# Performance work log

Hardware: AMD Instinct MI355X
Metric: run time of the kernel (lower is better)

## Reference

```python
import jax, jax.numpy as jnp
import numpy as np

N = 100_000   # number of sparse points
C = 128       # channels
K3 = 27       # 3x3x3 kernel offsets


def sparse_conv(x, nbr, W, b):
    """Minkowski-style sparse conv: gather-GEMM-scatter.
    x:   [N, Cin] point features
    nbr: [N, K3] neighbor index per kernel offset; index N -> missing (zero row)
    W:   [K3, Cin, Cout], b: [Cout]
    """
    x_pad = jnp.concatenate([x, jnp.zeros((1, x.shape[1]), x.dtype)], axis=0)

    def step(acc, wk_nk):
        Wk, nk = wk_nk                      # Wk: [Cin,Cout], nk: [N]
        return acc + x_pad[nk] @ Wk, None   # gather + GEMM, accumulate

    acc0 = jnp.broadcast_to(b, (x.shape[0], W.shape[2])).astype(x.dtype)
    acc, _ = jax.lax.scan(step, acc0, (W, nbr.T))
    return acc


def setup_inputs() -> dict:
    key = jax.random.key(0)
    ks = jax.random.split(key, 12)
    Ch = C // 2

    def w(k, shape, fan_in):
        return jax.random.normal(k, shape, dtype=jnp.float32) / np.sqrt(fan_in)

    x = jax.random.normal(ks[0], (N, C), dtype=jnp.float32)
    # neighbor map; value N means "no neighbor" (maps to zero-padded row)
    nbr = jax.random.randint(ks[1], (N, K3), 0, N + 1, dtype=jnp.int32)

    return {
        "x": x,
        "nbr": nbr,
        "W00": w(ks[2], (K3, C, Ch), K3 * C),   # conv0_0: kxkxk, C -> C/2
        "b00": jnp.zeros((Ch,), jnp.float32),
        "W01": w(ks[3], (K3, Ch, Ch), K3 * Ch),  # conv0_1: kxkxk, C/2 -> C/2
        "b01": jnp.zeros((Ch,), jnp.float32),
        "W10": w(ks[4], (C, Ch), C),             # conv1_0: 1x1x1, C -> C/2
        "b10": jnp.zeros((Ch,), jnp.float32),
        "W11": w(ks[5], (K3, Ch, Ch), K3 * Ch),  # conv1_1: kxkxk, C/2 -> C/2
        "b11": jnp.zeros((Ch,), jnp.float32),
        "W12": w(ks[6], (Ch, Ch), Ch),           # conv1_2: 1x1x1, C/2 -> C/2
        "b12": jnp.zeros((Ch,), jnp.float32),
    }


def reference(x, nbr, W00, b00, W01, b01, W10, b10, W11, b11, W12, b12):
    # branch 0: conv -> relu -> conv
    h0 = jax.nn.relu(sparse_conv(x, nbr, W00, b00))
    out0 = sparse_conv(h0, nbr, W01, b01)
    # branch 1: 1x1 conv -> relu -> conv -> relu -> 1x1 conv
    h1 = jax.nn.relu(x @ W10 + b10)
    h1 = jax.nn.relu(sparse_conv(h1, nbr, W11, b11))
    out1 = h1 @ W12 + b12
    # concat channels, residual add
    return jnp.concatenate([out0, out1], axis=1) + x
```

## Files before the change

kernel.cpp:

```cpp
#include <hip/hip_runtime.h>
#include <hip/hip_bf16.h>
#include <stdint.h>

typedef __bf16 bf16x8 __attribute__((ext_vector_type(8)));
typedef float  f32x4  __attribute__((ext_vector_type(4)));

#define MFMA(A, B, C) __builtin_amdgcn_mfma_f32_16x16x32_bf16((A), (B), (C), 0, 0, 0)

#define LDS_BARRIER() asm volatile("s_waitcnt lgkmcnt(0)\n\ts_barrier" ::: "memory")

static __device__ __forceinline__ unsigned short f2b(float f) {
    union { float f; unsigned int u; } v; v.f = f;
    return (unsigned short)((v.u + 0x7FFFu + ((v.u >> 16) & 1u)) >> 16);
}

static __device__ __forceinline__ bf16x8 perm_frag(int sel, bf16x8 D) {
    union { bf16x8 v; int d[4]; } u, r;
    u.v = D;
#pragma unroll
    for (int w = 0; w < 4; ++w) r.d[w] = __builtin_amdgcn_ds_bpermute(sel, u.d[w]);
    return r.v;
}

__global__ __launch_bounds__(256) void convert_kernel(
    const float* __restrict__ x, unsigned short* __restrict__ xb,
    unsigned short* __restrict__ hb, int N) {
    long long i = (long long)blockIdx.x * blockDim.x + threadIdx.x;
    long long base = i * 4;
    long long nx = (long long)N * 128;
    long long total = nx + 128;
    if (base >= total) return;
    if (base < nx) {
        float4 v = *(const float4*)(x + base);
        ushort4 o;
        o.x = f2b(v.x); o.y = f2b(v.y); o.z = f2b(v.z); o.w = f2b(v.w);
        *(ushort4*)(xb + base) = o;
    } else {
        ushort4 z = make_ushort4(0, 0, 0, 0);
        *(ushort4*)(xb + base) = z;
        *(ushort4*)(hb + base) = z;
    }
}

__global__ __launch_bounds__(256) void pack_kernel(
    const float* __restrict__ W00, const float* __restrict__ W01,
    const float* __restrict__ W10, const float* __restrict__ W11,
    const float* __restrict__ W12,
    unsigned short* __restrict__ wp00, unsigned short* __restrict__ wpC,
    unsigned short* __restrict__ wp10, unsigned short* __restrict__ wp12) {
    int g = blockIdx.x * blockDim.x + threadIdx.x;
    const float* W; int cinSteps; int which;
    if (g < 27648)      { W = W00; cinSteps = 4; which = 0; }
    else if (g < 41472) { g -= 27648; W = W01; cinSteps = 2; which = 1; }
    else if (g < 55296) { g -= 41472; W = W11; cinSteps = 2; which = 2; }
    else if (g < 56320) { g -= 55296; W = W10; cinSteps = 4; which = 3; }
    else if (g < 56832) { g -= 56320; W = W12; cinSteps = 2; which = 4; }
    else return;
    int lane = g & 63;
    int st   = g >> 6;
    int t    = st & 3;
    int s    = st >> 2;
    int q = lane >> 4, n16 = lane & 15;
    int k    = s / cinSteps;
    int cinb = (s % cinSteps) * 32;
    int Cin  = cinSteps * 32;
    int cout = t * 16 + n16;
    unsigned short o[8];
#pragma unroll
    for (int j = 0; j < 8; ++j) {
        float v = W[(size_t)(k * Cin + cinb + q * 8 + j) * 64 + cout];
        o[j] = f2b(v);
    }
    unsigned short* dst;
    if (which == 0)      dst = wp00 + (size_t)g * 8;
    else if (which == 1) dst = wpC + (size_t)k * 8192 +
                               ((size_t)(((s & 1) * 4 + t) * 64 + lane)) * 8;
    else if (which == 2) dst = wpC + (size_t)k * 8192 + 4096 +
                               ((size_t)(((s & 1) * 4 + t) * 64 + lane)) * 8;
    else if (which == 3) dst = wp10 + (size_t)g * 8;
    else                 dst = wp12 + (size_t)g * 8;
    *(ushort4*)(dst)     = make_ushort4(o[0], o[1], o[2], o[3]);
    *(ushort4*)(dst + 4) = make_ushort4(o[4], o[5], o[6], o[7]);
}

__global__ __launch_bounds__(256, 2) void passB_kernel(
    const unsigned short* __restrict__ xb, const int* __restrict__ nbr,
    const unsigned short* __restrict__ wp00, const unsigned short* __restrict__ wp10,
    const float* __restrict__ b00, const float* __restrict__ b10,
    unsigned short* __restrict__ hb, int N, int* __restrict__ ctr, int nstrips) {
    __shared__ __align__(16) unsigned short bbuf[2][8192];
    __shared__ int lds_idx[128 * 27];
    __shared__ int sstrip;
    int tid = threadIdx.x;
    int lane = tid & 63;
    int wv   = tid >> 6;
    int q = lane >> 4, n16 = lane & 15;
    int rowq = lane >> 2, chunk = lane & 3;
    int sel = (n16 * 4 + q) * 4;

    for (;;) {
        if (tid == 0) sstrip = atomicAdd(ctr, 1);
        __syncthreads();
        int strip = sstrip;
        if (strip >= nstrips) break;
        int rowbase = strip * 128 + wv * 32;

        int4 br[4];
#pragma unroll
        for (int j = 0; j < 4; ++j) br[j] = *(const int4*)(wp00 + j * 2048 + tid * 8);
        {
            long long gbase = (long long)strip * 128 * 27;
            long long lim = (long long)N * 27 - 1;
            for (int i = tid; i < 3456; i += 256) {
                long long gi = gbase + i; if (gi > lim) gi = lim;
                lds_idx[i] = nbr[gi];
            }
        }
#pragma unroll
        for (int j = 0; j < 4; ++j) *(int4*)(&bbuf[0][j * 2048 + tid * 8]) = br[j];
        __syncthreads();

        f32x4 acc0[2][4];
        f32x4 acc1[2][4];
#pragma unroll
        for (int rs = 0; rs < 2; ++rs)
#pragma unroll
            for (int t = 0; t < 4; ++t) { acc0[rs][t] = (f32x4)0.f; acc1[rs][t] = (f32x4)0.f; }

        int idxb0 = (wv * 32 + rowq) * 27;
        int idxb1 = (wv * 32 + 16 + rowq) * 27;
        int own0 = min(rowbase + rowq, N - 1);
        int own1 = min(rowbase + 16 + rowq, N - 1);

        int ia = lds_idx[idxb0], ib = lds_idx[idxb1];
        bf16x8 D0[4], D1[4];
        {
            const unsigned short* p0 = xb + (size_t)ia * 128 + chunk * 8;
            const unsigned short* p1 = xb + (size_t)ib * 128 + chunk * 8;
#pragma unroll
            for (int s2 = 0; s2 < 4; ++s2) {
                D0[s2] = *(const bf16x8*)(p0 + s2 * 32);
                D1[s2] = *(const bf16x8*)(p1 + s2 * 32);
            }
        }

        for (int k = 0; k < 27; ++k) {
            int buf = k & 1;
            if (k < 26) {
                const unsigned short* src = wp00 + (size_t)(k + 1) * 8192;
#pragma unroll
                for (int j = 0; j < 4; ++j) br[j] = *(const int4*)(src + j * 2048 + tid * 8);
            }
            int ian = (k + 1 < 27) ? lds_idx[idxb0 + k + 1] : own0;
            int ibn = (k + 1 < 27) ? lds_idx[idxb1 + k + 1] : own1;
            bf16x8 D0n[4], D1n[4];
            {
                const unsigned short* p0 = xb + (size_t)ian * 128 + chunk * 8;
                const unsigned short* p1 = xb + (size_t)ibn * 128 + chunk * 8;
#pragma unroll
                for (int s2 = 0; s2 < 4; ++s2) {
                    D0n[s2] = *(const bf16x8*)(p0 + s2 * 32);
                    D1n[s2] = *(const bf16x8*)(p1 + s2 * 32);
                }
            }
            const unsigned short* lb = &bbuf[buf][0];
#pragma unroll
            for (int s2 = 0; s2 < 4; ++s2) {
                bf16x8 A0 = perm_frag(sel, D0[s2]);
                bf16x8 A1 = perm_frag(sel, D1[s2]);
#pragma unroll
                for (int t = 0; t < 4; ++t) {
                    bf16x8 B = *(const bf16x8*)(lb + (s2 * 4 + t) * 512 + lane * 8);
                    acc0[0][t] = MFMA(A0, B, acc0[0][t]);
                    acc0[1][t] = MFMA(A1, B, acc0[1][t]);
                }
            }
            if (k < 26) {
#pragma unroll
                for (int j = 0; j < 4; ++j)
                    *(int4*)(&bbuf[buf ^ 1][j * 2048 + tid * 8]) = br[j];
            }
#pragma unroll
            for (int s2 = 0; s2 < 4; ++s2) { D0[s2] = D0n[s2]; D1[s2] = D1n[s2]; }
            LDS_BARRIER();
        }

#pragma unroll
        for (int s2 = 0; s2 < 4; ++s2) {
            bf16x8 A0 = perm_frag(sel, D0[s2]);
            bf16x8 A1 = perm_frag(sel, D1[s2]);
#pragma unroll
            for (int t = 0; t < 4; ++t) {
                bf16x8 B = *(const bf16x8*)(wp10 + s2 * 2048 + t * 512 + lane * 8);
                acc1[0][t] = MFMA(A0, B, acc1[0][t]);
                acc1[1][t] = MFMA(A1, B, acc1[1][t]);
            }
        }

#pragma unroll
        for (int rs = 0; rs < 2; ++rs)
#pragma unroll
            for (int t = 0; t < 4; ++t) {
                int col = t * 16 + n16;
                float bb0 = b00[col], bb1 = b10[col];
#pragma unroll
                for (int r = 0; r < 4; ++r) {
                    int row = rowbase + rs * 16 + q * 4 + r;
                    if (row < N) {
                        hb[(size_t)row * 128 + col]      = f2b(fmaxf(acc0[rs][t][r] + bb0, 0.f));
                        hb[(size_t)row * 128 + 64 + col] = f2b(fmaxf(acc1[rs][t][r] + bb1, 0.f));
                    }
                }
            }
        __syncthreads();
    }
}

__global__ __launch_bounds__(256, 2) void passC_kernel(
    const unsigned short* __restrict__ hb, const int* __restrict__ nbr,
    const float* __restrict__ x,
    const unsigned short* __restrict__ wpC, const unsigned short* __restrict__ wp12,
    const float* __restrict__ b01, const float* __restrict__ b11,
    const float* __restrict__ b12, float* __restrict__ out, int N,
    int* __restrict__ ctr, int nstrips) {
    __shared__ __align__(16) unsigned short bbuf[2][8192];
    __shared__ int lds_idx[128 * 27];
    __shared__ int sstrip;
    int tid = threadIdx.x;
    int lane = tid & 63;
    int wv   = tid >> 6;
    int q = lane >> 4, n16 = lane & 15;
    int rowq = lane >> 2, chunk = lane & 3;
    int sel = (n16 * 4 + q) * 4;

    for (;;) {
        if (tid == 0) sstrip = atomicAdd(ctr, 1);
        __syncthreads();
        int strip = sstrip;
        if (strip >= nstrips) break;
        int rowbase = strip * 128 + wv * 32;

        int4 br[4];
#pragma unroll
        for (int j = 0; j < 4; ++j) br[j] = *(const int4*)(wpC + j * 2048 + tid * 8);
        {
            long long gbase = (long long)strip * 128 * 27;
            long long lim = (long long)N * 27 - 1;
            for (int i = tid; i < 3456; i += 256) {
                long long gi = gbase + i; if (gi > lim) gi = lim;
                lds_idx[i] = nbr[gi];
            }
        }
#pragma unroll
        for (int j = 0; j < 4; ++j) *(int4*)(&bbuf[0][j * 2048 + tid * 8]) = br[j];
        __syncthreads();

        f32x4 accO0[2][4];
        f32x4 accT[2][4];
#pragma unroll
        for (int rs = 0; rs < 2; ++rs)
#pragma unroll
            for (int t = 0; t < 4; ++t) { accO0[rs][t] = (f32x4)0.f; accT[rs][t] = (f32x4)0.f; }

        int idxb0 = (wv * 32 + rowq) * 27;
        int idxb1 = (wv * 32 + 16 + rowq) * 27;

        int ia = lds_idx[idxb0], ib = lds_idx[idxb1];
        bf16x8 DA0[2], DC0[2], DA1[2], DC1[2];
        {
            const unsigned short* p0 = hb + (size_t)ia * 128 + chunk * 8;
            const unsigned short* p1 = hb + (size_t)ib * 128 + chunk * 8;
#pragma unroll
            for (int s2 = 0; s2 < 2; ++s2) {
                DA0[s2] = *(const bf16x8*)(p0 + s2 * 32);
                DC0[s2] = *(const bf16x8*)(p0 + 64 + s2 * 32);
                DA1[s2] = *(const bf16x8*)(p1 + s2 * 32);
                DC1[s2] = *(const bf16x8*)(p1 + 64 + s2 * 32);
            }
        }

        for (int k = 0; k < 27; ++k) {
            int buf = k & 1;
            if (k < 26) {
                const unsigned short* src = wpC + (size_t)(k + 1) * 8192;
#pragma unroll
                for (int j = 0; j < 4; ++j) br[j] = *(const int4*)(src + j * 2048 + tid * 8);
            }
            bf16x8 DA0n[2], DC0n[2], DA1n[2], DC1n[2];
            if (k < 26) {
                int ian = lds_idx[idxb0 + k + 1];
                int ibn = lds_idx[idxb1 + k + 1];
                const unsigned short* p0 = hb + (size_t)ian * 128 + chunk * 8;
                const unsigned short* p1 = hb + (size_t)ibn * 128 + chunk * 8;
#pragma unroll
                for (int s2 = 0; s2 < 2; ++s2) {
                    DA0n[s2] = *(const bf16x8*)(p0 + s2 * 32);
                    DC0n[s2] = *(const bf16x8*)(p0 + 64 + s2 * 32);
                    DA1n[s2] = *(const bf16x8*)(p1 + s2 * 32);
                    DC1n[s2] = *(const bf16x8*)(p1 + 64 + s2 * 32);
                }
            }
            const unsigned short* lb = &bbuf[buf][0];
#pragma unroll
            for (int s2 = 0; s2 < 2; ++s2) {
                bf16x8 A0 = perm_frag(sel, DA0[s2]);
                bf16x8 A1 = perm_frag(sel, DA1[s2]);
#pragma unroll
                for (int t = 0; t < 4; ++t) {
                    bf16x8 B = *(const bf16x8*)(lb + (s2 * 4 + t) * 512 + lane * 8);
                    accO0[0][t] = MFMA(A0, B, accO0[0][t]);
                    accO0[1][t] = MFMA(A1, B, accO0[1][t]);
                }
                bf16x8 C0 = perm_frag(sel, DC0[s2]);
                bf16x8 C1 = perm_frag(sel, DC1[s2]);
#pragma unroll
                for (int t = 0; t < 4; ++t) {
                    bf16x8 B2 = *(const bf16x8*)(lb + 4096 + (s2 * 4 + t) * 512 + lane * 8);
                    accT[0][t] = MFMA(C0, B2, accT[0][t]);
                    accT[1][t] = MFMA(C1, B2, accT[1][t]);
                }
            }
            if (k < 26) {
#pragma unroll
                for (int j = 0; j < 4; ++j)
                    *(int4*)(&bbuf[buf ^ 1][j * 2048 + tid * 8]) = br[j];
#pragma unroll
                for (int s2 = 0; s2 < 2; ++s2) {
                    DA0[s2] = DA0n[s2]; DC0[s2] = DC0n[s2];
                    DA1[s2] = DA1n[s2]; DC1[s2] = DC1n[s2];
                }
            }
            LDS_BARRIER();
        }

        unsigned short* scratch = &bbuf[0][0];
        unsigned short* myl = scratch + wv * 2304;
#pragma unroll
        for (int rs = 0; rs < 2; ++rs)
#pragma unroll
            for (int t = 0; t < 4; ++t) {
                int col = t * 16 + n16;
                float bo = b01[col], bt = b11[col];
#pragma unroll
                for (int r = 0; r < 4; ++r) {
                    int row = rowbase + rs * 16 + q * 4 + r;
                    if (row < N) {
                        float xv = __builtin_nontemporal_load(x + (size_t)row * 128 + col);
                        __builtin_nontemporal_store(accO0[rs][t][r] + bo + xv,
                                                    out + (size_t)row * 128 + col);
                    }
                    float tv = fmaxf(accT[rs][t][r] + bt, 0.f);
                    myl[(rs * 16 + q * 4 + r) * 72 + col] = f2b(tv);
                }
            }

        f32x4 accO1[2][4];
#pragma unroll
        for (int rs = 0; rs < 2; ++rs)
#pragma unroll
            for (int t = 0; t < 4; ++t) accO1[rs][t] = (f32x4)0.f;
#pragma unroll
        for (int s2 = 0; s2 < 2; ++s2) {
            bf16x8 A0 = *(const bf16x8*)(myl + n16 * 72 + s2 * 32 + q * 8);
            bf16x8 A1 = *(const bf16x8*)(myl + (16 + n16) * 72 + s2 * 32 + q * 8);
#pragma unroll
            for (int t = 0; t < 4; ++t) {
                bf16x8 B = *(const bf16x8*)(wp12 + s2 * 2048 + t * 512 + lane * 8);
                accO1[0][t] = MFMA(A0, B, accO1[0][t]);
                accO1[1][t] = MFMA(A1, B, accO1[1][t]);
            }
        }
#pragma unroll
        for (int rs = 0; rs < 2; ++rs)
#pragma unroll
            for (int t = 0; t < 4; ++t) {
                int col = t * 16 + n16;
                float bo = b12[col];
#pragma unroll
                for (int r = 0; r < 4; ++r) {
                    int row = rowbase + rs * 16 + q * 4 + r;
                    if (row < N) {
                        float xv = __builtin_nontemporal_load(x + (size_t)row * 128 + 64 + col);
                        __builtin_nontemporal_store(accO1[rs][t][r] + bo + xv,
                                                    out + (size_t)row * 128 + 64 + col);
                    }
                }
            }
        __syncthreads();
    }
}

extern "C" void kernel_launch(void* const* d_in, const int* in_sizes, int n_in,
                              void* d_out, int out_size, void* d_ws, size_t ws_size,
                              hipStream_t stream) {
    const float* x   = (const float*)d_in[0];
    const int*   nbr = (const int*)d_in[1];
    const float* W00 = (const float*)d_in[2];
    const float* b00 = (const float*)d_in[3];
    const float* W01 = (const float*)d_in[4];
    const float* b01 = (const float*)d_in[5];
    const float* W10 = (const float*)d_in[6];
    const float* b10 = (const float*)d_in[7];
    const float* W11 = (const float*)d_in[8];
    const float* b11 = (const float*)d_in[9];
    const float* W12 = (const float*)d_in[10];
    const float* b12 = (const float*)d_in[11];
    float* out = (float*)d_out;
    int N = in_sizes[0] / 128;

    char* ws = (char*)d_ws;
    size_t cur = 0;
    unsigned short* xb  = (unsigned short*)(ws + cur); cur += (size_t)(N + 1) * 128 * 2;
    unsigned short* hb  = (unsigned short*)(ws + cur); cur += (size_t)(N + 1) * 128 * 2;
    unsigned short* wp00 = (unsigned short*)(ws + cur); cur += 27648 * 8 * 2;
    unsigned short* wpC  = (unsigned short*)(ws + cur); cur += (size_t)27 * 8192 * 2;
    unsigned short* wp10 = (unsigned short*)(ws + cur); cur += 8192 * 2;
    unsigned short* wp12 = (unsigned short*)(ws + cur); cur += 4096 * 2;
    cur = (cur + 255) & ~(size_t)255;
    int* ctrs = (int*)(ws + cur); cur += 256;

    hipMemsetAsync(ctrs, 0, 8, stream);
    long long cvt_groups = ((long long)N * 128 + 128) / 4;
    int cvt_blocks = (int)((cvt_groups + 255) / 256);
    convert_kernel<<<cvt_blocks, 256, 0, stream>>>(x, xb, hb, N);
    pack_kernel<<<222, 256, 0, stream>>>(W00, W01, W10, W11, W12,
                                         wp00, wpC, wp10, wp12);
    int nstrips = (N + 127) / 128;
    passB_kernel<<<768, 256, 0, stream>>>(xb, nbr, wp00, wp10, b00, b10, hb, N,
                                          ctrs + 0, nstrips);
    passC_kernel<<<768, 256, 0, stream>>>(hb, nbr, x, wpC, wp12,
                                          b01, b11, b12, out, N,
                                          ctrs + 1, nstrips);
}
```

Measured before the change: 414.4 us.

## Drop persistent atomic scheduler, use one block per strip, remove bpermute shuffles

Replaces the persistent-block work queue (atomic counter plus memset) with a plain grid of one block per 128-row strip, and raises launch bounds to 3 blocks per CU. Each lane now gathers neighbor rows directly in the MFMA A-operand layout (row = n16, k-chunk = q), so the ds_bpermute fragment shuffles are no longer needed. This cuts per-iteration LDS permute traffic and the scheduler overhead. The cost is that each 16-lane group now reads 16 different rows per load, giving less contiguous gathers and more blocks to launch, and the tighter register budget could cause spills.

```diff
diff --git a/kernel.cpp b/kernel.cpp
--- a/kernel.cpp
+++ b/kernel.cpp
@@ -12,14 +12,6 @@
 static __device__ __forceinline__ unsigned short f2b(float f) {
     union { float f; unsigned int u; } v; v.f = f;
     return (unsigned short)((v.u + 0x7FFFu + ((v.u >> 16) & 1u)) >> 16);
-}
-
-static __device__ __forceinline__ bf16x8 perm_frag(int sel, bf16x8 D) {
-    union { bf16x8 v; int d[4]; } u, r;
-    u.v = D;
-#pragma unroll
-    for (int w = 0; w < 4; ++w) r.d[w] = __builtin_amdgcn_ds_bpermute(sel, u.d[w]);
-    return r.v;
 }
 
 __global__ __launch_bounds__(256) void convert_kernel(
@@ -83,311 +75,280 @@
     *(ushort4*)(dst + 4) = make_ushort4(o[4], o[5], o[6], o[7]);
 }
 
-__global__ __launch_bounds__(256, 2) void passB_kernel(
+__global__ __launch_bounds__(256, 3) void passB_kernel(
     const unsigned short* __restrict__ xb, const int* __restrict__ nbr,
     const unsigned short* __restrict__ wp00, const unsigned short* __restrict__ wp10,
     const float* __restrict__ b00, const float* __restrict__ b10,
-    unsigned short* __restrict__ hb, int N, int* __restrict__ ctr, int nstrips) {
+    unsigned short* __restrict__ hb, int N) {
     __shared__ __align__(16) unsigned short bbuf[2][8192];
     __shared__ int lds_idx[128 * 27];
-    __shared__ int sstrip;
-    int tid = threadIdx.x;
-    int lane = tid & 63;
-    int wv   = tid >> 6;
-    int q = lane >> 4, n16 = lane & 15;
-    int rowq = lane >> 2, chunk = lane & 3;
-    int sel = (n16 * 4 + q) * 4;
-
-    for (;;) {
-        if (tid == 0) sstrip = atomicAdd(ctr, 1);
-        __syncthreads();
-        int strip = sstrip;
-        if (strip >= nstrips) break;
-        int rowbase = strip * 128 + wv * 32;
-
-        int4 br[4];
-#pragma unroll
-        for (int j = 0; j < 4; ++j) br[j] = *(const int4*)(wp00 + j * 2048 + tid * 8);
+    const int tid  = threadIdx.x;
+    const int lane = tid & 63;
+    const int wv   = tid >> 6;
+    const int q = lane >> 4, n16 = lane & 15;
+    const int rowbase = blockIdx.x * 128 + wv * 32;
+
+    int4 br[4];
+#pragma unroll
+    for (int j = 0; j < 4; ++j) br[j] = *(const int4*)(wp00 + j * 2048 + tid * 8);
+    {
+        long long gbase = (long long)blockIdx.x * 128 * 27;
+        long long lim = (long long)N * 27 - 1;
+        for (int i = tid; i < 3456; i += 256) {
+            long long gi = gbase + i; if (gi > lim) gi = lim;
+            lds_idx[i] = nbr[gi];
+        }
+    }
+#pragma unroll
+    for (int j = 0; j < 4; ++j) *(int4*)(&bbuf[0][j * 2048 + tid * 8]) = br[j];
+    __syncthreads();
+
+    f32x4 acc0[2][4];
+    f32x4 acc1[2][4];
+#pragma unroll
+    for (int rs = 0; rs < 2; ++rs)
+#pragma unroll
+        for (int t = 0; t < 4; ++t) { acc0[rs][t] = (f32x4)0.f; acc1[rs][t] = (f32x4)0.f; }
+
+    const int idxb0 = (wv * 32 + n16) * 27;
+    const int idxb1 = (wv * 32 + 16 + n16) * 27;
+    const int own0 = min(rowbase + n16, N - 1);
+    const int own1 = min(rowbase + 16 + n16, N - 1);
+
+    int ia = lds_idx[idxb0], ib = lds_idx[idxb1];
+    bf16x8 D0[4], D1[4];
+    {
+        const unsigned short* p0 = xb + (size_t)ia * 128 + q * 8;
+        const unsigned short* p1 = xb + (size_t)ib * 128 + q * 8;
+#pragma unroll
+        for (int s2 = 0; s2 < 4; ++s2) {
+            D0[s2] = *(const bf16x8*)(p0 + s2 * 32);
+            D1[s2] = *(const bf16x8*)(p1 + s2 * 32);
+        }
+    }
+
+    for (int k = 0; k < 27; ++k) {
+        int buf = k & 1;
+        if (k < 26) {
+            const unsigned short* src = wp00 + (size_t)(k + 1) * 8192;
+#pragma unroll
+            for (int j = 0; j < 4; ++j) br[j] = *(const int4*)(src + j * 2048 + tid * 8);
+        }
+        int ian = (k + 1 < 27) ? lds_idx[idxb0 + k + 1] : own0;
+        int ibn = (k + 1 < 27) ? lds_idx[idxb1 + k + 1] : own1;
+        bf16x8 D0n[4], D1n[4];
         {
-            long long gbase = (long long)strip * 128 * 27;
-            long long lim = (long long)N * 27 - 1;
-            for (int i = tid; i < 3456; i += 256) {
-                long long gi = gbase + i; if (gi > lim) gi = lim;
-                lds_idx[i] = nbr[gi];
-            }
-        }
-#pragma unroll
-        for (int j = 0; j < 4; ++j) *(int4*)(&bbuf[0][j * 2048 + tid * 8]) = br[j];
-        __syncthreads();
-
-        f32x4 acc0[2][4];
-        f32x4 acc1[2][4];
-#pragma unroll
-        for (int rs = 0; rs < 2; ++rs)
-#pragma unroll
-            for (int t = 0; t < 4; ++t) { acc0[rs][t] = (f32x4)0.f; acc1[rs][t] = (f32x4)0.f; }
-
-        int idxb0 = (wv * 32 + rowq) * 27;
-        int idxb1 = (wv * 32 + 16 + rowq) * 27;
-        int own0 = min(rowbase + rowq, N - 1);
-        int own1 = min(rowbase + 16 + rowq, N - 1);
-
-        int ia = lds_idx[idxb0], ib = lds_idx[idxb1];
-        bf16x8 D0[4], D1[4];
-        {
-            const unsigned short* p0 = xb + (size_t)ia * 128 + chunk * 8;
-            const unsigned short* p1 = xb + (size_t)ib * 128 + chunk * 8;
+            const unsigned short* p0 = xb + (size_t)ian * 128 + q * 8;
+            const unsigned short* p1 = xb + (size_t)ibn * 128 + q * 8;
 #pragma unroll
             for (int s2 = 0; s2 < 4; ++s2) {
-                D0[s2] = *(const bf16x8*)(p0 + s2 * 32);
-                D1[s2] = *(const bf16x8*)(p1 + s2 * 32);
-            }
-        }
-
-        for (int k = 0; k < 27; ++k) {
-            int buf = k & 1;
-            if (k < 26) {
-                const unsigned short* src = wp00 + (size_t)(k + 1) * 8192;
-#pragma unroll
-                for (int j = 0; j < 4; ++j) br[j] = *(const int4*)(src + j * 2048 + tid * 8);
-            }
-            int ian = (k + 1 < 27) ? lds_idx[idxb0 + k + 1] : own0;
-            int ibn = (k + 1 < 27) ? lds_idx[idxb1 + k + 1] : own1;
-            bf16x8 D0n[4], D1n[4];
-            {
-                const unsigned short* p0 = xb + (size_t)ian * 128 + chunk * 8;
-                const unsigned short* p1 = xb + (size_t)ibn * 128 + chunk * 8;
-#pragma unroll
-                for (int s2 = 0; s2 < 4; ++s2) {
-                    D0n[s2] = *(const bf16x8*)(p0 + s2 * 32);
-                    D1n[s2] = *(const bf16x8*)(p1 + s2 * 32);
+                D0n[s2] = *(const bf16x8*)(p0 + s2 * 32);
+                D1n[s2] = *(const bf16x8*)(p1 + s2 * 32);
+            }
+        }
+        const unsigned short* lb = &bbuf[buf][0];
+#pragma unroll
+        for (int s2 = 0; s2 < 4; ++s2) {
+#pragma unroll
+            for (int t = 0; t < 4; ++t) {
+                bf16x8 B = *(const bf16x8*)(lb + (s2 * 4 + t) * 512 + lane * 8);
+                acc0[0][t] = MFMA(D0[s2], B, acc0[0][t]);
+                acc0[1][t] = MFMA(D1[s2], B, acc0[1][t]);
+            }
+        }
+        if (k < 26) {
+#pragma unroll
+            for (int j = 0; j < 4; ++j)
+                *(int4*)(&bbuf[buf ^ 1][j * 2048 + tid * 8]) = br[j];
+        }
+#pragma unroll
+        for (int s2 = 0; s2 < 4; ++s2) { D0[s2] = D0n[s2]; D1[s2] = D1n[s2]; }
+        LDS_BARRIER();
+    }
+
+#pragma unroll
+    for (int s2 = 0; s2 < 4; ++s2) {
+#pragma unroll
+        for (int t = 0; t < 4; ++t) {
+            bf16x8 B = *(const bf16x8*)(wp10 + s2 * 2048 + t * 512 + lane * 8);
+            acc1[0][t] = MFMA(D0[s2], B, acc1[0][t]);
+            acc1[1][t] = MFMA(D1[s2], B, acc1[1][t]);
+        }
+    }
+
+#pragma unroll
+    for (int rs = 0; rs < 2; ++rs)
+#pragma unroll
+        for (int t = 0; t < 4; ++t) {
+            int col = t * 16 + n16;
+            float bb0 = b00[col], bb1 = b10[col];
+#pragma unroll
+            for (int r = 0; r < 4; ++r) {
+                int row = rowbase + rs * 16 + q * 4 + r;
+                if (row < N) {
+                    hb[(size_t)row * 128 + col]      = f2b(fmaxf(acc0[rs][t][r] + bb0, 0.f));
+                    hb[(size_t)row * 128 + 64 + col] = f2b(fmaxf(acc1[rs][t][r] + bb1, 0.f));
                 }
             }
-            const unsigned short* lb = &bbuf[buf][0];
-#pragma unroll
-            for (int s2 = 0; s2 < 4; ++s2) {
-                bf16x8 A0 = perm_frag(sel, D0[s2]);
-                bf16x8 A1 = perm_frag(sel, D1[s2]);
-#pragma unroll
-                for (int t = 0; t < 4; ++t) {
-                    bf16x8 B = *(const bf16x8*)(lb + (s2 * 4 + t) * 512 + lane * 8);
-                    acc0[0][t] = MFMA(A0, B, acc0[0][t]);
-                    acc0[1][t] = MFMA(A1, B, acc0[1][t]);
-                }
-            }
-            if (k < 26) {
-#pragma unroll
-                for (int j = 0; j < 4; ++j)
-                    *(int4*)(&bbuf[buf ^ 1][j * 2048 + tid * 8]) = br[j];
-            }
-#pragma unroll
-            for (int s2 = 0; s2 < 4; ++s2) { D0[s2] = D0n[s2]; D1[s2] = D1n[s2]; }
-            LDS_BARRIER();
-        }
-
-#pragma unroll
-        for (int s2 = 0; s2 < 4; ++s2) {
-            bf16x8 A0 = perm_frag(sel, D0[s2]);
-            bf16x8 A1 = perm_frag(sel, D1[s2]);
-#pragma unroll
-            for (int t = 0; t < 4; ++t) {
-                bf16x8 B = *(const bf16x8*)(wp10 + s2 * 2048 + t * 512 + lane * 8);
-                acc1[0][t] = MFMA(A0, B, acc1[0][t]);
-                acc1[1][t] = MFMA(A1, B, acc1[1][t]);
-            }
-        }
-
-#pragma unroll
-        for (int rs = 0; rs < 2; ++rs)
-#pragma unroll
-            for (int t = 0; t < 4; ++t) {
-                int col = t * 16 + n16;
-                float bb0 = b00[col], bb1 = b10[col];
-#pragma unroll
-                for (int r = 0; r < 4; ++r) {
-                    int row = rowbase + rs * 16 + q * 4 + r;
-                    if (row < N) {
-                        hb[(size_t)row * 128 + col]      = f2b(fmaxf(acc0[rs][t][r] + bb0, 0.f));
-                        hb[(size_t)row * 128 + 64 + col] = f2b(fmaxf(acc1[rs][t][r] + bb1, 0.f));
-                    }
-                }
-            }
-        __syncthreads();
-    }
-}
-
-__global__ __launch_bounds__(256, 2) void passC_kernel(
+        }
+}
+
+__global__ __launch_bounds__(256, 3) void passC_kernel(
     const unsigned short* __restrict__ hb, const int* __restrict__ nbr,
     const float* __restrict__ x,
     const unsigned short* __restrict__ wpC, const unsigned short* __restrict__ wp12,
     const float* __restrict__ b01, const float* __restrict__ b11,
-    const float* __restrict__ b12, float* __restrict__ out, int N,
-    int* __restrict__ ctr, int nstrips) {
+    const float* __restrict__ b12, float* __restrict__ out, int N) {
     __shared__ __align__(16) unsigned short bbuf[2][8192];
     __shared__ int lds_idx[128 * 27];
-    __shared__ int sstrip;
-    int tid = threadIdx.x;
-    int lane = tid & 63;
-    int wv   = tid >> 6;
-    int q = lane >> 4, n16 = lane & 15;
-    int rowq = lane >> 2, chunk = lane & 3;
-    int sel = (n16 * 4 + q) * 4;
-
-    for (;;) {
-        if (tid == 0) sstrip = atomicAdd(ctr, 1);
-        __syncthreads();
-        int strip = sstrip;
-        if (strip >= nstrips) break;
-        int rowbase = strip * 128 + wv * 32;
-
-        int4 br[4];
-#pragma unroll
-        for (int j = 0; j < 4; ++j) br[j] = *(const int4*)(wpC + j * 2048 + tid * 8);
-        {
-            long long gbase = (long long)strip * 128 * 27;
-            long long lim = (long long)N * 27 - 1;
-            for (int i = tid; i < 3456; i += 256) {
-                long long gi = gbase + i; if (gi > lim) gi = lim;
-                lds_idx[i] = nbr[gi];
-            }
-        }
-#pragma unroll
-        for (int j = 0; j < 4; ++j) *(int4*)(&bbuf[0][j * 2048 + tid * 8]) = br[j];
-        __syncthreads();
-
-        f32x4 accO0[2][4];
-        f32x4 accT[2][4];
-#pragma unroll
-        for (int rs = 0; rs < 2; ++rs)
-#pragma unroll
-            for (int t = 0; t < 4; ++t) { accO0[rs][t] = (f32x4)0.f; accT[rs][t] = (f32x4)0.f; }
-
-        int idxb0 = (wv * 32 + rowq) * 27;
-        int idxb1 = (wv * 32 + 16 + rowq) * 27;
-
-        int ia = lds_idx[idxb0], ib = lds_idx[idxb1];
-        bf16x8 DA0[2], DC0[2], DA1[2], DC1[2];
-        {
-            const unsigned short* p0 = hb + (size_t)ia * 128 + chunk * 8;
-            const unsigned short* p1 = hb + (size_t)ib * 128 + chunk * 8;
+    const int tid  = threadIdx.x;
+    const int lane = tid & 63;
+    const int wv   = tid >> 6;
+    const int q = lane >> 4, n16 = lane & 15;
+    const int rowbase = blockIdx.x * 128 + wv * 32;
+
+    int4 br[4];
+#pragma unroll
+    for (int j = 0; j < 4; ++j) br[j] = *(const int4*)(wpC + j * 2048 + tid * 8);
+    {
+        long long gbase = (long long)blockIdx.x * 128 * 27;
+        long long lim = (long long)N * 27 - 1;
+        for (int i = tid; i < 3456; i += 256) {
+            long long gi = gbase + i; if (gi > lim) gi = lim;
+            lds_idx[i] = nbr[gi];
+        }
+    }
+#pragma unroll
+    for (int j = 0; j < 4; ++j) *(int4*)(&bbuf[0][j * 2048 + tid * 8]) = br[j];
+    __syncthreads();
+
+    f32x4 accO0[2][4];
+    f32x4 accT[2][4];
+#pragma unroll
+    for (int rs = 0; rs < 2; ++rs)
+#pragma unroll
+        for (int t = 0; t < 4; ++t) { accO0[rs][t] = (f32x4)0.f; accT[rs][t] = (f32x4)0.f; }
+
+    const int idxb0 = (wv * 32 + n16) * 27;
+    const int idxb1 = (wv * 32 + 16 + n16) * 27;
+
+    int ia = lds_idx[idxb0], ib = lds_idx[idxb1];
+    bf16x8 DA0[2], DC0[2], DA1[2], DC1[2];
+    {
+        const unsigned short* p0 = hb + (size_t)ia * 128 + q * 8;
+        const unsigned short* p1 = hb + (size_t)ib * 128 + q * 8;
+#pragma unroll
+        for (int s2 = 0; s2 < 2; ++s2) {
+            DA0[s2] = *(const bf16x8*)(p0 + s2 * 32);
+            DC0[s2] = *(const bf16x8*)(p0 + 64 + s2 * 32);
+            DA1[s2] = *(const bf16x8*)(p1 + s2 * 32);
+            DC1[s2] = *(const bf16x8*)(p1 + 64 + s2 * 32);
+        }
+    }
+
+    for (int k = 0; k < 27; ++k) {
+        int buf = k & 1;
+        if (k < 26) {
+            const unsigned short* src = wpC + (size_t)(k + 1) * 8192;
+#pragma unroll
+            for (int j = 0; j < 4; ++j) br[j] = *(const int4*)(src + j * 2048 + tid * 8);
+        }
+        bf16x8 DA0n[2], DC0n[2], DA1n[2], DC1n[2];
+        if (k < 26) {
+            int ian = lds_idx[idxb0 + k + 1];
+            int ibn = lds_idx[idxb1 + k + 1];
+            const unsigned short* p0 = hb + (size_t)ian * 128 + q * 8;
+            const unsigned short* p1 = hb + (size_t)ibn * 128 + q * 8;
 #pragma unroll
             for (int s2 = 0; s2 < 2; ++s2) {
-                DA0[s2] = *(const bf16x8*)(p0 + s2 * 32);
-                DC0[s2] = *(const bf16x8*)(p0 + 64 + s2 * 32);
-                DA1[s2] = *(const bf16x8*)(p1 + s2 * 32);
-                DC1[s2] = *(const bf16x8*)(p1 + 64 + s2 * 32);
-            }
-        }
-
-        for (int k = 0; k < 27; ++k) {
-            int buf = k & 1;
-            if (k < 26) {
-                const unsigned short* src = wpC + (size_t)(k + 1) * 8192;
-#pragma unroll
-                for (int j = 0; j < 4; ++j) br[j] = *(const int4*)(src + j * 2048 + tid * 8);
-            }
-            bf16x8 DA0n[2], DC0n[2], DA1n[2], DC1n[2];
-            if (k < 26) {
-                int ian = lds_idx[idxb0 + k + 1];
-                int ibn = lds_idx[idxb1 + k + 1];
-                const unsigned short* p0 = hb + (size_t)ian * 128 + chunk * 8;
-                const unsigned short* p1 = hb + (size_t)ibn * 128 + chunk * 8;
-#pragma unroll
-                for (int s2 = 0; s2 < 2; ++s2) {
-                    DA0n[s2] = *(const bf16x8*)(p0 + s2 * 32);
-                    DC0n[s2] = *(const bf16x8*)(p0 + 64 + s2 * 32);
-                    DA1n[s2] = *(const bf16x8*)(p1 + s2 * 32);
-                    DC1n[s2] = *(const bf16x8*)(p1 + 64 + s2 * 32);
+                DA0n[s2] = *(const bf16x8*)(p0 + s2 * 32);
+                DC0n[s2] = *(const bf16x8*)(p0 + 64 + s2 * 32);
+                DA1n[s2] = *(const bf16x8*)(p1 + s2 * 32);
+                DC1n[s2] = *(const bf16x8*)(p1 + 64 + s2 * 32);
+            }
+        }
+        const unsigned short* lb = &bbuf[buf][0];
+#pragma unroll
+        for (int s2 = 0; s2 < 2; ++s2) {
+#pragma unroll
+            for (int t = 0; t < 4; ++t) {
+                bf16x8 B = *(const bf16x8*)(lb + (s2 * 4 + t) * 512 + lane * 8);
+                accO0[0][t] = MFMA(DA0[s2], B, accO0[0][t]);
+                accO0[1][t] = MFMA(DA1[s2], B, accO0[1][t]);
+            }
+#pragma unroll
+            for (int t = 0; t < 4; ++t) {
+                bf16x8 B2 = *(const bf16x8*)(lb + 4096 + (s2 * 4 + t) * 512 + lane * 8);
+                accT[0][t] = MFMA(DC0[s2], B2, accT[0][t]);
+                accT[1][t] = MFMA(DC1[s2], B2, accT[1][t]);
+            }
+        }
+        if (k < 26) {
+#pragma unroll
+            for (int j = 0; j < 4; ++j)
+                *(int4*)(&bbuf[buf ^ 1][j * 2048 + tid * 8]) = br[j];
+#pragma unroll
+            for (int s2 = 0; s2 < 2; ++s2) {
+                DA0[s2] = DA0n[s2]; DC0[s2] = DC0n[s2];
+                DA1[s2] = DA1n[s2]; DC1[s2] = DC1n[s2];
+            }
+        }
+        LDS_BARRIER();
+    }
+
+    unsigned short* scratch = &bbuf[0][0];
+    unsigned short* myl = scratch + wv * 2304;
+#pragma unroll
+    for (int rs = 0; rs < 2; ++rs)
+#pragma unroll
+        for (int t = 0; t < 4; ++t) {
+            int col = t * 16 + n16;
+            float bo = b01[col], bt = b11[col];
+#pragma unroll
+            for (int r = 0; r < 4; ++r) {
+                int row = rowbase + rs * 16 + q * 4 + r;
+                if (row < N) {
+                    float xv = __builtin_nontemporal_load(x + (size_t)row * 128 + col);
+                    __builtin_nontemporal_store(accO0[rs][t][r] + bo + xv,
+                                                out + (size_t)row * 128 + col);
                 }
-            }
-            const unsigned short* lb = &bbuf[buf][0];
-#pragma unroll
-            for (int s2 = 0; s2 < 2; ++s2) {
-                bf16x8 A0 = perm_frag(sel, DA0[s2]);
-                bf16x8 A1 = perm_frag(sel, DA1[s2]);
-#pragma unroll
-                for (int t = 0; t < 4; ++t) {
-                    bf16x8 B = *(const bf16x8*)(lb + (s2 * 4 + t) * 512 + lane * 8);
-                    accO0[0][t] = MFMA(A0, B, accO0[0][t]);
-                    accO0[1][t] = MFMA(A1, B, accO0[1][t]);
+                float tv = fmaxf(accT[rs][t][r] + bt, 0.f);
+                myl[(rs * 16 + q * 4 + r) * 72 + col] = f2b(tv);
+            }
+        }
+
+    f32x4 accO1[2][4];
+#pragma unroll
+    for (int rs = 0; rs < 2; ++rs)
+#pragma unroll
+        for (int t = 0; t < 4; ++t) accO1[rs][t] = (f32x4)0.f;
+#pragma unroll
+    for (int s2 = 0; s2 < 2; ++s2) {
+        bf16x8 A0 = *(const bf16x8*)(myl + n16 * 72 + s2 * 32 + q * 8);
+        bf16x8 A1 = *(const bf16x8*)(myl + (16 + n16) * 72 + s2 * 32 + q * 8);
+#pragma unroll
+        for (int t = 0; t < 4; ++t) {
+            bf16x8 B = *(const bf16x8*)(wp12 + s2 * 2048 + t * 512 + lane * 8);
+            accO1[0][t] = MFMA(A0, B, accO1[0][t]);
+            accO1[1][t] = MFMA(A1, B, accO1[1][t]);
+        }
+    }
+#pragma unroll
+    for (int rs = 0; rs < 2; ++rs)
+#pragma unroll
+        for (int t = 0; t < 4; ++t) {
+            int col = t * 16 + n16;
+            float bo = b12[col];
+#pragma unroll
+            for (int r = 0; r < 4; ++r) {
+                int row = rowbase + rs * 16 + q * 4 + r;
+                if (row < N) {
+                    float xv = __builtin_nontemporal_load(x + (size_t)row * 128 + 64 + col);
+                    __builtin_nontemporal_store(accO1[rs][t][r] + bo + xv,
+                                                out + (size_t)row * 128 + 64 + col);
                 }
-                bf16x8 C0 = perm_frag(sel, DC0[s2]);
-                bf16x8 C1 = perm_frag(sel, DC1[s2]);
-#pragma unroll
-                for (int t = 0; t < 4; ++t) {
-                    bf16x8 B2 = *(const bf16x8*)(lb + 4096 + (s2 * 4 + t) * 512 + lane * 8);
-                    accT[0][t] = MFMA(C0, B2, accT[0][t]);
-                    accT[1][t] = MFMA(C1, B2, accT[1][t]);
-                }
-            }
-            if (k < 26) {
-#pragma unroll
-                for (int j = 0; j < 4; ++j)
-                    *(int4*)(&bbuf[buf ^ 1][j * 2048 + tid * 8]) = br[j];
-#pragma unroll
-                for (int s2 = 0; s2 < 2; ++s2) {
-                    DA0[s2] = DA0n[s2]; DC0[s2] = DC0n[s2];
-                    DA1[s2] = DA1n[s2]; DC1[s2] = DC1n[s2];
-                }
-            }
-            LDS_BARRIER();
-        }
-
-        unsigned short* scratch = &bbuf[0][0];
-        unsigned short* myl = scratch + wv * 2304;
-#pragma unroll
-        for (int rs = 0; rs < 2; ++rs)
-#pragma unroll
-            for (int t = 0; t < 4; ++t) {
-                int col = t * 16 + n16;
-                float bo = b01[col], bt = b11[col];
-#pragma unroll
-                for (int r = 0; r < 4; ++r) {
-                    int row = rowbase + rs * 16 + q * 4 + r;
-                    if (row < N) {
-                        float xv = __builtin_nontemporal_load(x + (size_t)row * 128 + col);
-                        __builtin_nontemporal_store(accO0[rs][t][r] + bo + xv,
-                                                    out + (size_t)row * 128 + col);
-                    }
-                    float tv = fmaxf(accT[rs][t][r] + bt, 0.f);
-                    myl[(rs * 16 + q * 4 + r) * 72 + col] = f2b(tv);
-                }
-            }
-
-        f32x4 accO1[2][4];
-#pragma unroll
-        for (int rs = 0; rs < 2; ++rs)
-#pragma unroll
-            for (int t = 0; t < 4; ++t) accO1[rs][t] = (f32x4)0.f;
-#pragma unroll
-        for (int s2 = 0; s2 < 2; ++s2) {
-            bf16x8 A0 = *(const bf16x8*)(myl + n16 * 72 + s2 * 32 + q * 8);
-            bf16x8 A1 = *(const bf16x8*)(myl + (16 + n16) * 72 + s2 * 32 + q * 8);
-#pragma unroll
-            for (int t = 0; t < 4; ++t) {
-                bf16x8 B = *(const bf16x8*)(wp12 + s2 * 2048 + t * 512 + lane * 8);
-                accO1[0][t] = MFMA(A0, B, accO1[0][t]);
-                accO1[1][t] = MFMA(A1, B, accO1[1][t]);
-            }
-        }
-#pragma unroll
-        for (int rs = 0; rs < 2; ++rs)
-#pragma unroll
-            for (int t = 0; t < 4; ++t) {
-                int col = t * 16 + n16;
-                float bo = b12[col];
-#pragma unroll
-                for (int r = 0; r < 4; ++r) {
-                    int row = rowbase + rs * 16 + q * 4 + r;
-                    if (row < N) {
-                        float xv = __builtin_nontemporal_load(x + (size_t)row * 128 + 64 + col);
-                        __builtin_nontemporal_store(accO1[rs][t][r] + bo + xv,
-                                                    out + (size_t)row * 128 + 64 + col);
-                    }
-                }
-            }
-        __syncthreads();
-    }
+            }
+        }
 }
 
 extern "C" void kernel_launch(void* const* d_in, const int* in_sizes, int n_in,
@@ -416,19 +377,14 @@
     unsigned short* wpC  = (unsigned short*)(ws + cur); cur += (size_t)27 * 8192 * 2;
     unsigned short* wp10 = (unsigned short*)(ws + cur); cur += 8192 * 2;
     unsigned short* wp12 = (unsigned short*)(ws + cur); cur += 4096 * 2;
-    cur = (cur + 255) & ~(size_t)255;
-    int* ctrs = (int*)(ws + cur); cur += 256;
-
-    hipMemsetAsync(ctrs, 0, 8, stream);
+
     long long cvt_groups = ((long long)N * 128 + 128) / 4;
     int cvt_blocks = (int)((cvt_groups + 255) / 256);
     convert_kernel<<<cvt_blocks, 256, 0, stream>>>(x, xb, hb, N);
     pack_kernel<<<222, 256, 0, stream>>>(W00, W01, W10, W11, W12,
                                          wp00, wpC, wp10, wp12);
     int nstrips = (N + 127) / 128;
-    passB_kernel<<<768, 256, 0, stream>>>(xb, nbr, wp00, wp10, b00, b10, hb, N,
-                                          ctrs + 0, nstrips);
-    passC_kernel<<<768, 256, 0, stream>>>(hb, nbr, x, wpC, wp12,
-                                          b01, b11, b12, out, N,
-                                          ctrs + 1, nstrips);
-}
+    passB_kernel<<<nstrips, 256, 0, stream>>>(xb, nbr, wp00, wp10, b00, b10, hb, N);
+    passC_kernel<<<nstrips, 256, 0, stream>>>(hb, nbr, x, wpC, wp12,
+                                              b01, b11, b12, out, N);
+}
```

Result: slower. 430.1 us (+3.8%).
